# Kernel optimization log

Measured on AMD Instinct MI355X. Metric: run time of the kernel, lower is better.

Reference implementation:

```python
import jax, jax.numpy as jnp
import numpy as np

B, N_MM, N_V, N_A = 2, 256, 64, 128
DIM, HEADS, ATTN_RATIO, MLP_RATIO = 1024, 16, 0.25, 4.0
INNER = int(DIM * ATTN_RATIO)          # 256
HID = int(DIM * MLP_RATIO)             # 4096
SCALE = (DIM // HEADS) ** -0.5         # faithful to source: uses dim//num_heads
EPS = 1e-5


def setup_inputs() -> dict:
    key = jax.random.key(0)
    ks = jax.random.split(key, 16)
    s = 0.02
    return {
        "xmm": jax.random.normal(ks[0], (B, N_MM, DIM), jnp.float32),
        "xv": jax.random.normal(ks[1], (B, N_V, DIM), jnp.float32),
        "xa": jax.random.normal(ks[2], (B, N_A, DIM), jnp.float32),
        "ln_mm_w": jnp.ones((DIM,), jnp.float32),
        "ln_mm_b": jnp.zeros((DIM,), jnp.float32),
        "ln_v_w": jnp.ones((DIM,), jnp.float32),
        "ln_v_b": jnp.zeros((DIM,), jnp.float32),
        "ln_a_w": jnp.ones((DIM,), jnp.float32),
        "ln_a_b": jnp.zeros((DIM,), jnp.float32),
        "Wq": jax.random.normal(ks[3], (DIM, INNER), jnp.float32) * s,
        "Wkv": jax.random.normal(ks[4], (2 * DIM, 2 * INNER), jnp.float32) * s,
        "Wproj": jax.random.normal(ks[5], (INNER, DIM), jnp.float32) * s,
        "bproj": jnp.zeros((DIM,), jnp.float32),
        "ln_mlp_w": jnp.ones((DIM,), jnp.float32),
        "ln_mlp_b": jnp.zeros((DIM,), jnp.float32),
        "W1": jax.random.normal(ks[6], (DIM, HID), jnp.float32) * s,
        "b1": jnp.zeros((HID,), jnp.float32),
        "W2": jax.random.normal(ks[7], (HID, DIM), jnp.float32) * s,
        "b2": jnp.zeros((DIM,), jnp.float32),
    }


def _ln(x, w, b):
    m = x.mean(-1, keepdims=True)
    v = ((x - m) ** 2).mean(-1, keepdims=True)
    return (x - m) / jnp.sqrt(v + EPS) * w + b


def reference(xmm, xv, xa, ln_mm_w, ln_mm_b, ln_v_w, ln_v_b, ln_a_w, ln_a_b,
              Wq, Wkv, Wproj, bproj, ln_mlp_w, ln_mlp_b, W1, b1, W2, b2):
    hd = INNER // HEADS
    src_mm = _ln(xmm, ln_mm_w, ln_mm_b)
    src_v = _ln(xv, ln_v_w, ln_v_b)
    src_a = _ln(xa, ln_a_w, ln_a_b)

    # kv(x_va) where x_va = cat([xv broadcast over N_a, xa broadcast over N_v], -1).
    # Equivalent to projecting each stream separately and broadcast-adding:
    kv_v = src_v @ Wkv[:DIM]            # [B, N_v, 2*INNER]
    kv_a = src_a @ Wkv[DIM:]            # [B, N_a, 2*INNER]
    kv = kv_v[:, :, None, :] + kv_a[:, None, :, :]          # [B, N_v, N_a, 2*INNER]
    kv = kv.reshape(B, N_V * N_A, 2, HEADS, hd)
    k = kv[:, :, 0].transpose(0, 2, 1, 3)                   # [B, H, N_va, hd]
    v = kv[:, :, 1].transpose(0, 2, 1, 3)

    q = (src_mm @ Wq).reshape(B, N_MM, HEADS, hd).transpose(0, 2, 1, 3)

    attn = jnp.einsum('bhqd,bhkd->bhqk', q, k) * SCALE
    attn = jax.nn.softmax(attn, axis=-1)
    out = jnp.einsum('bhqk,bhkd->bhqd', attn, v)
    out = out.transpose(0, 2, 1, 3).reshape(B, N_MM, INNER)
    out = out @ Wproj + bproj

    xmm = xmm + out
    h = _ln(xmm, ln_mlp_w, ln_mlp_b)
    h = jax.nn.gelu(h @ W1 + b1, approximate=False) @ W2 + b2
    return xmm + h
```

## Files before the change

### kernel.cpp

```cpp
#include <hip/hip_runtime.h>
#include <hip/hip_bf16.h>
#include <math.h>


typedef unsigned short ushort_t;
typedef __attribute__((ext_vector_type(8))) __bf16 bf16x8;
typedef __attribute__((ext_vector_type(4))) float f32x4;

#define DEVFN static __device__ __forceinline__

DEVFN float bf2f(ushort_t u) {
    return __uint_as_float(((unsigned int)u) << 16);
}
DEVFN ushort_t f2bf(float f) {
    unsigned int x = __float_as_uint(f);
    unsigned int r = x + 0x7FFFu + ((x >> 16) & 1u);
    return (ushort_t)(r >> 16);
}
DEVFN bf16x8 asbf8(uint4 v) {
    union { uint4 u; bf16x8 b; } c;
    c.u = v;
    return c.b;
}
DEVFN void unpack8(uint4 dv, float* dst) {
    unsigned int ws[4] = {dv.x, dv.y, dv.z, dv.w};
#pragma unroll
    for (int i = 0; i < 4; i++) {
        dst[2 * i] = __uint_as_float(ws[i] << 16);
        dst[2 * i + 1] = __uint_as_float(ws[i] & 0xFFFF0000u);
    }
}

template <int TM, int K>
DEVFN void wave_acc(const ushort_t* __restrict__ A, int lda,
                    const ushort_t* __restrict__ B, int ldb, int m0, int n0,
                    int lane, f32x4 (&acc)[TM][4]) {
    int quad = lane >> 4, l16 = lane & 15;
    const ushort_t* Ap = A + (size_t)(m0 + l16) * lda + quad * 8;
    const ushort_t* Bp = B + (size_t)(n0 + l16) * ldb + quad * 8;

    uint4 ra[TM], rb[4];
#pragma unroll
    for (int i = 0; i < TM; i++)
        ra[i] = *(const uint4*)(Ap + (size_t)i * 16 * lda);
#pragma unroll
    for (int j = 0; j < 4; j++)
        rb[j] = *(const uint4*)(Bp + (size_t)j * 16 * ldb);

#pragma unroll 2
    for (int k0 = 0; k0 < K; k0 += 32) {
        uint4 na[TM], nb[4];
        if (k0 + 32 < K) {
#pragma unroll
            for (int i = 0; i < TM; i++)
                na[i] = *(const uint4*)(Ap + (size_t)i * 16 * lda + k0 + 32);
#pragma unroll
            for (int j = 0; j < 4; j++)
                nb[j] = *(const uint4*)(Bp + (size_t)j * 16 * ldb + k0 + 32);
        }
#pragma unroll
        for (int i = 0; i < TM; i++) {
            bf16x8 af = asbf8(ra[i]);
#pragma unroll
            for (int j = 0; j < 4; j++)
                acc[i][j] = __builtin_amdgcn_mfma_f32_16x16x32_bf16(
                    af, asbf8(rb[j]), acc[i][j], 0, 0, 0);
        }
        if (k0 + 32 < K) {
#pragma unroll
            for (int i = 0; i < TM; i++) ra[i] = na[i];
#pragma unroll
            for (int j = 0; j < 4; j++) rb[j] = nb[j];
        }
    }
}

__global__ __launch_bounds__(64) void qkv_kernel(
    const ushort_t* __restrict__ xmmN, const ushort_t* __restrict__ xvN,
    const ushort_t* __restrict__ xaN, const ushort_t* __restrict__ Wqt,
    const ushort_t* __restrict__ Wkvt, ushort_t* __restrict__ qout,
    ushort_t* __restrict__ kvvb, ushort_t* __restrict__ kvab) {
    int id = blockIdx.x;
    int lane = threadIdx.x;
    const ushort_t *A, *B;
    ushort_t* C;
    int lda, ldb, ldc, m0, n0;
    if (id < 64) {
        A = xmmN; B = Wqt; C = qout; lda = 1024; ldb = 1024; ldc = 256;
        m0 = (id >> 2) * 32; n0 = (id & 3) * 64;
    } else if (id < 96) {
        int t = id - 64;
        A = xvN; B = Wkvt; C = kvvb; lda = 1024; ldb = 2048; ldc = 512;
        m0 = (t >> 3) * 32; n0 = (t & 7) * 64;
    } else {
        int t = id - 96;
        A = xaN; B = Wkvt + 1024; C = kvab; lda = 1024; ldb = 2048; ldc = 512;
        m0 = (t >> 3) * 32; n0 = (t & 7) * 64;
    }
    f32x4 acc[2][4];
#pragma unroll
    for (int i = 0; i < 2; i++)
#pragma unroll
        for (int j = 0; j < 4; j++) acc[i][j] = (f32x4){0.f, 0.f, 0.f, 0.f};
    wave_acc<2, 1024>(A, lda, B, ldb, m0, n0, lane, acc);

    int quad = lane >> 4, l16 = lane & 15;
#pragma unroll
    for (int i = 0; i < 2; i++)
#pragma unroll
        for (int j = 0; j < 4; j++) {
            int col = n0 + j * 16 + l16;
            int rbase = m0 + i * 16 + quad * 4;
#pragma unroll
            for (int rr = 0; rr < 4; rr++)
                C[(size_t)(rbase + rr) * ldc + col] = f2bf(acc[i][j][rr]);
        }
}

__global__ __launch_bounds__(64) void proj_kernel(
    const ushort_t* __restrict__ attnout, const ushort_t* __restrict__ Wprojt,
    const float* __restrict__ bproj, const float* __restrict__ xmm,
    const float* __restrict__ b2, float* __restrict__ y,
    float* __restrict__ outp, float* __restrict__ stats) {
    int id = blockIdx.x;
    int lane = threadIdx.x;
    int m0 = (id >> 4) * 32, n0 = (id & 15) * 64;
    f32x4 acc[2][4];
#pragma unroll
    for (int i = 0; i < 2; i++)
#pragma unroll
        for (int j = 0; j < 4; j++) acc[i][j] = (f32x4){0.f, 0.f, 0.f, 0.f};
    wave_acc<2, 256>(attnout, 256, Wprojt, 256, m0, n0, lane, acc);

    int quad = lane >> 4, l16 = lane & 15;
    float rs[2][4] = {{0.f, 0.f, 0.f, 0.f}, {0.f, 0.f, 0.f, 0.f}};
    float rq[2][4] = {{0.f, 0.f, 0.f, 0.f}, {0.f, 0.f, 0.f, 0.f}};
#pragma unroll
    for (int i = 0; i < 2; i++)
#pragma unroll
        for (int j = 0; j < 4; j++) {
            int col = n0 + j * 16 + l16;
            int rbase = m0 + i * 16 + quad * 4;
            float bv = bproj[col];
            float b2v = b2[col];
#pragma unroll
            for (int rr = 0; rr < 4; rr++) {
                int row = rbase + rr;
                float vv = acc[i][j][rr] + bv + xmm[(size_t)row * 1024 + col];
                y[(size_t)row * 1024 + col] = vv;
                outp[(size_t)row * 1024 + col] = vv + b2v;
                rs[i][rr] += vv;
                rq[i][rr] += vv * vv;
            }
        }
#pragma unroll
    for (int i = 0; i < 2; i++)
#pragma unroll
        for (int rr = 0; rr < 4; rr++) {
            float s = rs[i][rr], q = rq[i][rr];
            s += __shfl_xor(s, 1); q += __shfl_xor(q, 1);
            s += __shfl_xor(s, 2); q += __shfl_xor(q, 2);
            s += __shfl_xor(s, 4); q += __shfl_xor(q, 4);
            s += __shfl_xor(s, 8); q += __shfl_xor(q, 8);
            if (l16 == 0) {
                int row = m0 + i * 16 + quad * 4 + rr;
                atomicAdd(&stats[row], s);
                atomicAdd(&stats[512 + row], q);
            }
        }
}

__global__ __launch_bounds__(64) void mlp1_kernel(
    const ushort_t* __restrict__ h0, const ushort_t* __restrict__ W1t,
    const float* __restrict__ b1, ushort_t* __restrict__ g) {
    int id = blockIdx.x;
    int lane = threadIdx.x;
    int m0 = (id >> 6) * 64, n0 = (id & 63) * 64;
    f32x4 acc[4][4];
#pragma unroll
    for (int i = 0; i < 4; i++)
#pragma unroll
        for (int j = 0; j < 4; j++) acc[i][j] = (f32x4){0.f, 0.f, 0.f, 0.f};
    wave_acc<4, 1024>(h0, 1024, W1t, 1024, m0, n0, lane, acc);

    int quad = lane >> 4, l16 = lane & 15;
#pragma unroll
    for (int i = 0; i < 4; i++)
#pragma unroll
        for (int j = 0; j < 4; j++) {
            int col = n0 + j * 16 + l16;
            int rbase = m0 + i * 16 + quad * 4;
            float bv = b1[col];
#pragma unroll
            for (int rr = 0; rr < 4; rr++) {
                float vv = acc[i][j][rr] + bv;
                vv = 0.5f * vv * (1.f + erff(vv * 0.70710678118654752f));
                g[(size_t)(rbase + rr) * 4096 + col] = f2bf(vv);
            }
        }
}

__global__ __launch_bounds__(64) void mlp2_kernel(
    const ushort_t* __restrict__ g, const ushort_t* __restrict__ W2t,
    float* __restrict__ outp) {
    int id = blockIdx.x;
    int z = blockIdx.y;
    int lane = threadIdx.x;
    int m0 = (id >> 4) * 64, n0 = (id & 15) * 64;
    f32x4 acc[4][4];
#pragma unroll
    for (int i = 0; i < 4; i++)
#pragma unroll
        for (int j = 0; j < 4; j++) acc[i][j] = (f32x4){0.f, 0.f, 0.f, 0.f};
    wave_acc<4, 1024>(g + z * 1024, 4096, W2t + z * 1024, 4096, m0, n0, lane,
                      acc);

    int quad = lane >> 4, l16 = lane & 15;
#pragma unroll
    for (int i = 0; i < 4; i++)
#pragma unroll
        for (int j = 0; j < 4; j++) {
            int col = n0 + j * 16 + l16;
            int rbase = m0 + i * 16 + quad * 4;
#pragma unroll
            for (int rr = 0; rr < 4; rr++)
                atomicAdd(&outp[(size_t)(rbase + rr) * 1024 + col],
                          acc[i][j][rr]);
        }
}

__global__ __launch_bounds__(256) void ln_apply(
    const float* __restrict__ y, const float* __restrict__ stats,
    const float* __restrict__ w, const float* __restrict__ b,
    ushort_t* __restrict__ h0) {
    int row = blockIdx.x, tid = threadIdx.x;
    float s = stats[row], ss = stats[512 + row];
    float mean = s * (1.f / 1024.f);
    float rstd = rsqrtf(ss * (1.f / 1024.f) - mean * mean + 1e-5f);
    float4 v4 = ((const float4*)(y + (size_t)row * 1024))[tid];
    float4 w4 = ((const float4*)w)[tid];
    float4 b4 = ((const float4*)b)[tid];
    union { ushort_t u[4]; uint2 v; } pk;
    pk.u[0] = f2bf((v4.x - mean) * rstd * w4.x + b4.x);
    pk.u[1] = f2bf((v4.y - mean) * rstd * w4.y + b4.y);
    pk.u[2] = f2bf((v4.z - mean) * rstd * w4.z + b4.z);
    pk.u[3] = f2bf((v4.w - mean) * rstd * w4.w + b4.w);
    *(uint2*)(h0 + (size_t)row * 1024 + tid * 4) = pk.v;
}

struct LNSeg {
    const float* x; const float* w; const float* b; ushort_t* out; int start;
};
struct TDesc { const float* in; ushort_t* out; int R, C, nx, start; };

__global__ __launch_bounds__(256) void prep_kernel(LNSeg l0, LNSeg l1,
                                                   LNSeg l2, TDesc d0,
                                                   TDesc d1, TDesc d2,
                                                   TDesc d3, TDesc d4,
                                                   float* stats) {
    int id = blockIdx.x;
    int tid = threadIdx.x;
    if (id == 0) ((float4*)stats)[tid] = (float4){0.f, 0.f, 0.f, 0.f};

    if (id < 896) {
        const float *x, *w, *b; ushort_t* o; int start;
        if (id >= l2.start)      { x = l2.x; w = l2.w; b = l2.b; o = l2.out; start = l2.start; }
        else if (id >= l1.start) { x = l1.x; w = l1.w; b = l1.b; o = l1.out; start = l1.start; }
        else                     { x = l0.x; w = l0.w; b = l0.b; o = l0.out; start = 0; }
        int row = id - start;
        const float4* xr4 = (const float4*)(x + (size_t)row * 1024);
        float4 v4 = xr4[tid];
        float s = v4.x + v4.y + v4.z + v4.w;
        float ss = v4.x * v4.x + v4.y * v4.y + v4.z * v4.z + v4.w * v4.w;
#pragma unroll
        for (int off = 32; off > 0; off >>= 1) {
            s += __shfl_down(s, off);
            ss += __shfl_down(ss, off);
        }
        __shared__ float red[8];
        if ((tid & 63) == 0) {
            red[tid >> 6] = s;
            red[4 + (tid >> 6)] = ss;
        }
        __syncthreads();
        s = red[0] + red[1] + red[2] + red[3];
        ss = red[4] + red[5] + red[6] + red[7];
        float mean = s * (1.f / 1024.f);
        float var = ss * (1.f / 1024.f) - mean * mean;
        float rstd = rsqrtf(var + 1e-5f);
        const float4 w4 = ((const float4*)w)[tid];
        const float4 b4 = ((const float4*)b)[tid];
        union { ushort_t u[4]; uint2 v; } pk;
        pk.u[0] = f2bf((v4.x - mean) * rstd * w4.x + b4.x);
        pk.u[1] = f2bf((v4.y - mean) * rstd * w4.y + b4.y);
        pk.u[2] = f2bf((v4.z - mean) * rstd * w4.z + b4.z);
        pk.u[3] = f2bf((v4.w - mean) * rstd * w4.w + b4.w);
        *(uint2*)(o + (size_t)row * 1024 + tid * 4) = pk.v;
        return;
    }

    int t = id - 896;
    const float* in; ushort_t* out; int R, C, nx, start;
    if (t >= d4.start)      { in = d4.in; out = d4.out; R = d4.R; C = d4.C; nx = d4.nx; start = d4.start; }
    else if (t >= d3.start) { in = d3.in; out = d3.out; R = d3.R; C = d3.C; nx = d3.nx; start = d3.start; }
    else if (t >= d2.start) { in = d2.in; out = d2.out; R = d2.R; C = d2.C; nx = d2.nx; start = d2.start; }
    else if (t >= d1.start) { in = d1.in; out = d1.out; R = d1.R; C = d1.C; nx = d1.nx; start = d1.start; }
    else                    { in = d0.in; out = d0.out; R = d0.R; C = d0.C; nx = d0.nx; start = 0; }
    int tt = t - start;
    int bx = (tt % nx) * 64;
    int by = (tt / nx) * 64;
    __shared__ ushort_t tile[64 * 65];
    int r = tid >> 4, c4 = (tid & 15) * 4;
#pragma unroll
    for (int rr = 0; rr < 4; rr++) {
        int rl = r + rr * 16;
        float4 f = *(const float4*)(in + (size_t)(by + rl) * C + bx + c4);
        ushort_t* tr = tile + rl * 65 + c4;
        tr[0] = f2bf(f.x); tr[1] = f2bf(f.y);
        tr[2] = f2bf(f.z); tr[3] = f2bf(f.w);
    }
    __syncthreads();
#pragma unroll
    for (int rr = 0; rr < 4; rr++) {
        int orow = r + rr * 16;
        union { ushort_t u[4]; uint2 v; } pk;
#pragma unroll
        for (int j = 0; j < 4; j++) pk.u[j] = tile[(c4 + j) * 65 + orow];
        *(uint2*)(out + (size_t)(bx + orow) * R + by + c4) = pk.v;
    }
}

__global__ __launch_bounds__(256) void attn_kernel(
    const ushort_t* __restrict__ q, const ushort_t* __restrict__ kvv,
    const ushort_t* __restrict__ kva, ushort_t* __restrict__ out) {
    int bh = blockIdx.x;
    int b = bh >> 4, h = bh & 15;
    int tid = threadIdx.x;

    __shared__ float Kv[64][16], Vv[64][16], Ka[128][16], Va[128][16];
    {
        int row = tid >> 2, seg = (tid >> 1) & 1, half = tid & 1;
        const ushort_t* src =
            kvv + (size_t)(b * 64 + row) * 512 + seg * 256 + h * 16 + half * 8;
        float* dst = (seg ? Vv[row] : Kv[row]) + half * 8;
        unpack8(*(const uint4*)src, dst);
    }
#pragma unroll
    for (int t2 = 0; t2 < 2; t2++) {
        int t = tid + t2 * 256;
        int row = t >> 2, seg = (t >> 1) & 1, half = t & 1;
        const ushort_t* src =
            kva + (size_t)(b * 128 + row) * 512 + seg * 256 + h * 16 + half * 8;
        float* dst = (seg ? Va[row] : Ka[row]) + half * 8;
        unpack8(*(const uint4*)src, dst);
    }
    __syncthreads();

    int qlocal = tid >> 2;
    int dg = tid & 3;
    int qrow = blockIdx.y * 64 + qlocal;
    const ushort_t* qp = q + (size_t)(b * 256 + qrow) * 256 + h * 16 + dg * 4;
    uint2 qu = *(const uint2*)qp;
    float4 qv;
    qv.x = __uint_as_float(qu.x << 16) * 0.125f;
    qv.y = __uint_as_float(qu.x & 0xFFFF0000u) * 0.125f;
    qv.z = __uint_as_float(qu.y << 16) * 0.125f;
    qv.w = __uint_as_float(qu.y & 0xFFFF0000u) * 0.125f;

    const float4* Kv4 = (const float4*)Kv;
    const float4* Vv4 = (const float4*)Vv;
    const float4* Ka4 = (const float4*)Ka;
    const float4* Va4 = (const float4*)Va;

    float4 ov = {0.f, 0.f, 0.f, 0.f};
    float den = 0.f;
#pragma unroll 8
    for (int i = 0; i < 64; i++) {
        float4 kk = Kv4[i * 4 + dg];
        float part = qv.x * kk.x + qv.y * kk.y + qv.z * kk.z + qv.w * kk.w;
        part += __shfl_xor(part, 1);
        part += __shfl_xor(part, 2);
        float pe = __expf(part);
        den += pe;
        float4 vv = Vv4[i * 4 + dg];
        ov.x += pe * vv.x; ov.y += pe * vv.y;
        ov.z += pe * vv.z; ov.w += pe * vv.w;
    }
    float4 oa = {0.f, 0.f, 0.f, 0.f};
    float dena = 0.f;
#pragma unroll 8
    for (int i = 0; i < 128; i++) {
        float4 kk = Ka4[i * 4 + dg];
        float part = qv.x * kk.x + qv.y * kk.y + qv.z * kk.z + qv.w * kk.w;
        part += __shfl_xor(part, 1);
        part += __shfl_xor(part, 2);
        float pe = __expf(part);
        dena += pe;
        float4 vv = Va4[i * 4 + dg];
        oa.x += pe * vv.x; oa.y += pe * vv.y;
        oa.z += pe * vv.z; oa.w += pe * vv.w;
    }

    float rv = 1.f / den, ra = 1.f / dena;
    union { ushort_t u[4]; uint2 v; } pk;
    pk.u[0] = f2bf(ov.x * rv + oa.x * ra);
    pk.u[1] = f2bf(ov.y * rv + oa.y * ra);
    pk.u[2] = f2bf(ov.z * rv + oa.z * ra);
    pk.u[3] = f2bf(ov.w * rv + oa.w * ra);
    *(uint2*)(out + (size_t)(b * 256 + qrow) * 256 + h * 16 + dg * 4) = pk.v;
}

extern "C" void kernel_launch(void* const* d_in, const int* in_sizes, int n_in,
                              void* d_out, int out_size, void* d_ws,
                              size_t ws_size, hipStream_t stream) {
    const float* xmm = (const float*)d_in[0];
    const float* xv = (const float*)d_in[1];
    const float* xa = (const float*)d_in[2];
    const float* ln_mm_w = (const float*)d_in[3];
    const float* ln_mm_b = (const float*)d_in[4];
    const float* ln_v_w = (const float*)d_in[5];
    const float* ln_v_b = (const float*)d_in[6];
    const float* ln_a_w = (const float*)d_in[7];
    const float* ln_a_b = (const float*)d_in[8];
    const float* Wq = (const float*)d_in[9];
    const float* Wkv = (const float*)d_in[10];
    const float* Wproj = (const float*)d_in[11];
    const float* bproj = (const float*)d_in[12];
    const float* ln_mlp_w = (const float*)d_in[13];
    const float* ln_mlp_b = (const float*)d_in[14];
    const float* W1 = (const float*)d_in[15];
    const float* b1 = (const float*)d_in[16];
    const float* W2 = (const float*)d_in[17];
    const float* b2 = (const float*)d_in[18];
    float* outp = (float*)d_out;

    char* w = (char*)d_ws;
    ushort_t* xmmN = (ushort_t*)w;    w += 512 * 1024 * 2;
    ushort_t* xvN = (ushort_t*)w;     w += 128 * 1024 * 2;
    ushort_t* xaN = (ushort_t*)w;     w += 256 * 1024 * 2;
    ushort_t* Wqt = (ushort_t*)w;     w += 256 * 1024 * 2;
    ushort_t* Wkvt = (ushort_t*)w;    w += 512 * 2048 * 2;
    ushort_t* Wprojt = (ushort_t*)w;  w += 1024 * 256 * 2;
    ushort_t* W1t = (ushort_t*)w;     w += 4096 * 1024 * 2;
    ushort_t* W2t = (ushort_t*)w;     w += 1024 * 4096 * 2;
    ushort_t* qout = (ushort_t*)w;    w += 512 * 256 * 2;
    ushort_t* kvvb = (ushort_t*)w;    w += 128 * 512 * 2;
    ushort_t* kvab = (ushort_t*)w;    w += 256 * 512 * 2;
    ushort_t* attnout = (ushort_t*)w; w += 512 * 256 * 2;
    float* y = (float*)w;             w += 512 * 1024 * 4;
    ushort_t* h0 = (ushort_t*)w;      w += 512 * 1024 * 2;
    ushort_t* g = (ushort_t*)w;       w += 512 * 4096 * 2;
    float* stats = (float*)w;         w += 1024 * 4;

    LNSeg L0{xmm, ln_mm_w, ln_mm_b, xmmN, 0};
    LNSeg L1{xv, ln_v_w, ln_v_b, xvN, 512};
    LNSeg L2{xa, ln_a_w, ln_a_b, xaN, 640};
    TDesc T0{Wq, Wqt, 1024, 256, 4, 0};
    TDesc T1{Wkv, Wkvt, 2048, 512, 8, 64};
    TDesc T2{Wproj, Wprojt, 256, 1024, 16, 320};
    TDesc T3{W1, W1t, 1024, 4096, 64, 384};
    TDesc T4{W2, W2t, 4096, 1024, 16, 1408};
    prep_kernel<<<896 + 2432, 256, 0, stream>>>(L0, L1, L2, T0, T1, T2, T3,
                                                T4, stats);

    qkv_kernel<<<160, 64, 0, stream>>>(xmmN, xvN, xaN, Wqt, Wkvt, qout, kvvb,
                                       kvab);

    attn_kernel<<<dim3(32, 4), 256, 0, stream>>>(qout, kvvb, kvab, attnout);

    proj_kernel<<<256, 64, 0, stream>>>(attnout, Wprojt, bproj, xmm, b2, y,
                                        outp, stats);

    ln_apply<<<512, 256, 0, stream>>>(y, stats, ln_mlp_w, ln_mlp_b, h0);

    mlp1_kernel<<<512, 64, 0, stream>>>(h0, W1t, b1, g);

    mlp2_kernel<<<dim3(128, 4), 64, 0, stream>>>(g, W2t, outp);

    (void)in_sizes; (void)n_in; (void)out_size; (void)ws_size;
}
```

Measured before the change: 207.6 us.

## Double-buffer MFMA operand loads, shrink MLP tiles, rewrite weight transpose

The GEMM inner loop now keeps two register stages of A/B fragments and issues loads two K-steps ahead, giving memory latency more time to hide behind MFMAs. The MLP kernels drop from 64-row to 32-row tiles and launch twice as many single-wave blocks, trading more redundant weight reads for more parallelism. The weight transpose-and-convert in the prep kernel is replaced by a direct strided-gather version without shared memory: each thread packs 8 K-consecutive values into one 16-byte store, using more blocks. The two-stage buffers raise register pressure.

```diff
diff --git a/kernel.cpp b/kernel.cpp
--- a/kernel.cpp
+++ b/kernel.cpp
@@ -32,45 +32,58 @@
 }
 
 template <int TM, int K>
-DEVFN void wave_acc(const ushort_t* __restrict__ A, int lda,
-                    const ushort_t* __restrict__ B, int ldb, int m0, int n0,
-                    int lane, f32x4 (&acc)[TM][4]) {
+DEVFN void wave_acc2(const ushort_t* __restrict__ A, int lda,
+                     const ushort_t* __restrict__ B, int ldb, int m0, int n0,
+                     int lane, f32x4 (&acc)[TM][4]) {
     int quad = lane >> 4, l16 = lane & 15;
     const ushort_t* Ap = A + (size_t)(m0 + l16) * lda + quad * 8;
     const ushort_t* Bp = B + (size_t)(n0 + l16) * ldb + quad * 8;
 
-    uint4 ra[TM], rb[4];
+    uint4 a0[TM], b0[4], a1[TM], b1[4];
+#pragma unroll
+    for (int i = 0; i < TM; i++) a0[i] = *(const uint4*)(Ap + (size_t)i * 16 * lda);
+#pragma unroll
+    for (int j = 0; j < 4; j++) b0[j] = *(const uint4*)(Bp + (size_t)j * 16 * ldb);
 #pragma unroll
     for (int i = 0; i < TM; i++)
-        ra[i] = *(const uint4*)(Ap + (size_t)i * 16 * lda);
+        a1[i] = *(const uint4*)(Ap + (size_t)i * 16 * lda + 32);
 #pragma unroll
     for (int j = 0; j < 4; j++)
-        rb[j] = *(const uint4*)(Bp + (size_t)j * 16 * ldb);
-
-#pragma unroll 2
-    for (int k0 = 0; k0 < K; k0 += 32) {
-        uint4 na[TM], nb[4];
-        if (k0 + 32 < K) {
-#pragma unroll
-            for (int i = 0; i < TM; i++)
-                na[i] = *(const uint4*)(Ap + (size_t)i * 16 * lda + k0 + 32);
-#pragma unroll
-            for (int j = 0; j < 4; j++)
-                nb[j] = *(const uint4*)(Bp + (size_t)j * 16 * ldb + k0 + 32);
-        }
+        b1[j] = *(const uint4*)(Bp + (size_t)j * 16 * ldb + 32);
+
+#pragma unroll
+    for (int k0 = 0; k0 < K; k0 += 64) {
 #pragma unroll
         for (int i = 0; i < TM; i++) {
-            bf16x8 af = asbf8(ra[i]);
+            bf16x8 af = asbf8(a0[i]);
 #pragma unroll
             for (int j = 0; j < 4; j++)
                 acc[i][j] = __builtin_amdgcn_mfma_f32_16x16x32_bf16(
-                    af, asbf8(rb[j]), acc[i][j], 0, 0, 0);
-        }
-        if (k0 + 32 < K) {
-#pragma unroll
-            for (int i = 0; i < TM; i++) ra[i] = na[i];
-#pragma unroll
-            for (int j = 0; j < 4; j++) rb[j] = nb[j];
+                    af, asbf8(b0[j]), acc[i][j], 0, 0, 0);
+        }
+        if (k0 + 64 < K) {
+#pragma unroll
+            for (int i = 0; i < TM; i++)
+                a0[i] = *(const uint4*)(Ap + (size_t)i * 16 * lda + k0 + 64);
+#pragma unroll
+            for (int j = 0; j < 4; j++)
+                b0[j] = *(const uint4*)(Bp + (size_t)j * 16 * ldb + k0 + 64);
+        }
+#pragma unroll
+        for (int i = 0; i < TM; i++) {
+            bf16x8 af = asbf8(a1[i]);
+#pragma unroll
+            for (int j = 0; j < 4; j++)
+                acc[i][j] = __builtin_amdgcn_mfma_f32_16x16x32_bf16(
+                    af, asbf8(b1[j]), acc[i][j], 0, 0, 0);
+        }
+        if (k0 + 96 < K) {
+#pragma unroll
+            for (int i = 0; i < TM; i++)
+                a1[i] = *(const uint4*)(Ap + (size_t)i * 16 * lda + k0 + 96);
+#pragma unroll
+            for (int j = 0; j < 4; j++)
+                b1[j] = *(const uint4*)(Bp + (size_t)j * 16 * ldb + k0 + 96);
         }
     }
 }
@@ -102,7 +115,7 @@
     for (int i = 0; i < 2; i++)
 #pragma unroll
         for (int j = 0; j < 4; j++) acc[i][j] = (f32x4){0.f, 0.f, 0.f, 0.f};
-    wave_acc<2, 1024>(A, lda, B, ldb, m0, n0, lane, acc);
+    wave_acc2<2, 1024>(A, lda, B, ldb, m0, n0, lane, acc);
 
     int quad = lane >> 4, l16 = lane & 15;
 #pragma unroll
@@ -130,7 +143,7 @@
     for (int i = 0; i < 2; i++)
 #pragma unroll
         for (int j = 0; j < 4; j++) acc[i][j] = (f32x4){0.f, 0.f, 0.f, 0.f};
-    wave_acc<2, 256>(attnout, 256, Wprojt, 256, m0, n0, lane, acc);
+    wave_acc2<2, 256>(attnout, 256, Wprojt, 256, m0, n0, lane, acc);
 
     int quad = lane >> 4, l16 = lane & 15;
     float rs[2][4] = {{0.f, 0.f, 0.f, 0.f}, {0.f, 0.f, 0.f, 0.f}};
@@ -175,17 +188,17 @@
     const float* __restrict__ b1, ushort_t* __restrict__ g) {
     int id = blockIdx.x;
     int lane = threadIdx.x;
-    int m0 = (id >> 6) * 64, n0 = (id & 63) * 64;
-    f32x4 acc[4][4];
-#pragma unroll
-    for (int i = 0; i < 4; i++)
+    int m0 = (id >> 6) * 32, n0 = (id & 63) * 64;
+    f32x4 acc[2][4];
+#pragma unroll
+    for (int i = 0; i < 2; i++)
 #pragma unroll
         for (int j = 0; j < 4; j++) acc[i][j] = (f32x4){0.f, 0.f, 0.f, 0.f};
-    wave_acc<4, 1024>(h0, 1024, W1t, 1024, m0, n0, lane, acc);
+    wave_acc2<2, 1024>(h0, 1024, W1t, 1024, m0, n0, lane, acc);
 
     int quad = lane >> 4, l16 = lane & 15;
 #pragma unroll
-    for (int i = 0; i < 4; i++)
+    for (int i = 0; i < 2; i++)
 #pragma unroll
         for (int j = 0; j < 4; j++) {
             int col = n0 + j * 16 + l16;
@@ -206,18 +219,18 @@
     int id = blockIdx.x;
     int z = blockIdx.y;
     int lane = threadIdx.x;
-    int m0 = (id >> 4) * 64, n0 = (id & 15) * 64;
-    f32x4 acc[4][4];
-#pragma unroll
-    for (int i = 0; i < 4; i++)
+    int m0 = (id >> 4) * 32, n0 = (id & 15) * 64;
+    f32x4 acc[2][4];
+#pragma unroll
+    for (int i = 0; i < 2; i++)
 #pragma unroll
         for (int j = 0; j < 4; j++) acc[i][j] = (f32x4){0.f, 0.f, 0.f, 0.f};
-    wave_acc<4, 1024>(g + z * 1024, 4096, W2t + z * 1024, 4096, m0, n0, lane,
-                      acc);
+    wave_acc2<2, 1024>(g + z * 1024, 4096, W2t + z * 1024, 4096, m0, n0, lane,
+                       acc);
 
     int quad = lane >> 4, l16 = lane & 15;
 #pragma unroll
-    for (int i = 0; i < 4; i++)
+    for (int i = 0; i < 2; i++)
 #pragma unroll
         for (int j = 0; j < 4; j++) {
             int col = n0 + j * 16 + l16;
@@ -251,12 +264,11 @@
 struct LNSeg {
     const float* x; const float* w; const float* b; ushort_t* out; int start;
 };
-struct TDesc { const float* in; ushort_t* out; int R, C, nx, start; };
+struct TD { const float* in; ushort_t* out; int C; int K; int nkt; int start; };
 
 __global__ __launch_bounds__(256) void prep_kernel(LNSeg l0, LNSeg l1,
-                                                   LNSeg l2, TDesc d0,
-                                                   TDesc d1, TDesc d2,
-                                                   TDesc d3, TDesc d4,
+                                                   LNSeg l2, TD d0, TD d1,
+                                                   TD d2, TD d3, TD d4,
                                                    float* stats) {
     int id = blockIdx.x;
     int tid = threadIdx.x;
@@ -300,34 +312,21 @@
     }
 
     int t = id - 896;
-    const float* in; ushort_t* out; int R, C, nx, start;
-    if (t >= d4.start)      { in = d4.in; out = d4.out; R = d4.R; C = d4.C; nx = d4.nx; start = d4.start; }
-    else if (t >= d3.start) { in = d3.in; out = d3.out; R = d3.R; C = d3.C; nx = d3.nx; start = d3.start; }
-    else if (t >= d2.start) { in = d2.in; out = d2.out; R = d2.R; C = d2.C; nx = d2.nx; start = d2.start; }
-    else if (t >= d1.start) { in = d1.in; out = d1.out; R = d1.R; C = d1.C; nx = d1.nx; start = d1.start; }
-    else                    { in = d0.in; out = d0.out; R = d0.R; C = d0.C; nx = d0.nx; start = 0; }
+    const float* in; ushort_t* out; int C, K, nkt, start;
+    if (t >= d4.start)      { in = d4.in; out = d4.out; C = d4.C; K = d4.K; nkt = d4.nkt; start = d4.start; }
+    else if (t >= d3.start) { in = d3.in; out = d3.out; C = d3.C; K = d3.K; nkt = d3.nkt; start = d3.start; }
+    else if (t >= d2.start) { in = d2.in; out = d2.out; C = d2.C; K = d2.K; nkt = d2.nkt; start = d2.start; }
+    else if (t >= d1.start) { in = d1.in; out = d1.out; C = d1.C; K = d1.K; nkt = d1.nkt; start = d1.start; }
+    else                    { in = d0.in; out = d0.out; C = d0.C; K = d0.K; nkt = d0.nkt; start = 0; }
     int tt = t - start;
-    int bx = (tt % nx) * 64;
-    int by = (tt / nx) * 64;
-    __shared__ ushort_t tile[64 * 65];
-    int r = tid >> 4, c4 = (tid & 15) * 4;
-#pragma unroll
-    for (int rr = 0; rr < 4; rr++) {
-        int rl = r + rr * 16;
-        float4 f = *(const float4*)(in + (size_t)(by + rl) * C + bx + c4);
-        ushort_t* tr = tile + rl * 65 + c4;
-        tr[0] = f2bf(f.x); tr[1] = f2bf(f.y);
-        tr[2] = f2bf(f.z); tr[3] = f2bf(f.w);
-    }
-    __syncthreads();
-#pragma unroll
-    for (int rr = 0; rr < 4; rr++) {
-        int orow = r + rr * 16;
-        union { ushort_t u[4]; uint2 v; } pk;
-#pragma unroll
-        for (int j = 0; j < 4; j++) pk.u[j] = tile[(c4 + j) * 65 + orow];
-        *(uint2*)(out + (size_t)(bx + orow) * R + by + c4) = pk.v;
-    }
+    int kt = tt % nkt, nt = tt / nkt;
+    int n0 = nt * 64, k0 = kt * 32;
+    int nl = tid & 63, kc = tid >> 6;
+    const float* src = in + (size_t)(k0 + kc * 8) * C + n0 + nl;
+    union { ushort_t u[8]; uint4 v; } pk;
+#pragma unroll
+    for (int j = 0; j < 8; j++) pk.u[j] = f2bf(src[(size_t)j * C]);
+    *(uint4*)(out + (size_t)(n0 + nl) * K + k0 + kc * 8) = pk.v;
 }
 
 __global__ __launch_bounds__(256) void attn_kernel(
@@ -455,12 +454,12 @@
     LNSeg L0{xmm, ln_mm_w, ln_mm_b, xmmN, 0};
     LNSeg L1{xv, ln_v_w, ln_v_b, xvN, 512};
     LNSeg L2{xa, ln_a_w, ln_a_b, xaN, 640};
-    TDesc T0{Wq, Wqt, 1024, 256, 4, 0};
-    TDesc T1{Wkv, Wkvt, 2048, 512, 8, 64};
-    TDesc T2{Wproj, Wprojt, 256, 1024, 16, 320};
-    TDesc T3{W1, W1t, 1024, 4096, 64, 384};
-    TDesc T4{W2, W2t, 4096, 1024, 16, 1408};
-    prep_kernel<<<896 + 2432, 256, 0, stream>>>(L0, L1, L2, T0, T1, T2, T3,
+    TD T0{Wq, Wqt, 256, 1024, 32, 0};
+    TD T1{Wkv, Wkvt, 512, 2048, 64, 128};
+    TD T2{Wproj, Wprojt, 1024, 256, 8, 640};
+    TD T3{W1, W1t, 4096, 1024, 32, 768};
+    TD T4{W2, W2t, 1024, 4096, 128, 2816};
+    prep_kernel<<<896 + 4864, 256, 0, stream>>>(L0, L1, L2, T0, T1, T2, T3,
                                                 T4, stats);
 
     qkv_kernel<<<160, 64, 0, stream>>>(xmmN, xvN, xaN, Wqt, Wkvt, qout, kvvb,
@@ -473,9 +472,9 @@
 
     ln_apply<<<512, 256, 0, stream>>>(y, stats, ln_mlp_w, ln_mlp_b, h0);
 
-    mlp1_kernel<<<512, 64, 0, stream>>>(h0, W1t, b1, g);
-
-    mlp2_kernel<<<dim3(128, 4), 64, 0, stream>>>(g, W2t, outp);
+    mlp1_kernel<<<1024, 64, 0, stream>>>(h0, W1t, b1, g);
+
+    mlp2_kernel<<<dim3(256, 4), 64, 0, stream>>>(g, W2t, outp);
 
     (void)in_sizes; (void)n_in; (void)out_size; (void)ws_size;
 }
```

Result: slower. 222.9 us (+7.4%).
